# Kernel tuning notes

Measured on AMD Instinct MI355X. Metric: run time of the kernel, lower is better.

## Reference

```python
import jax, jax.numpy as jnp
import numpy as np

N_LSTM = 256
FEAT = 5
BATCH = 65536


def setup_inputs() -> dict:
    key = jax.random.key(0)
    ks = jax.random.split(key, 9)
    s = 1.0 / np.sqrt(N_LSTM)
    return {
        "seq_in": jax.random.normal(ks[0], (BATCH, 1, FEAT), dtype=jnp.float32),
        "h0": jax.random.normal(ks[1], (BATCH, N_LSTM), dtype=jnp.float32) * 0.1,
        "c0": jax.random.normal(ks[2], (BATCH, N_LSTM), dtype=jnp.float32) * 0.1,
        "W": jax.random.normal(ks[3], (FEAT, 4 * N_LSTM), dtype=jnp.float32) * s,
        "U": jax.random.normal(ks[4], (N_LSTM, 4 * N_LSTM), dtype=jnp.float32) * s,
        "b": jnp.zeros((4 * N_LSTM,), dtype=jnp.float32),
        "Wd": jax.random.normal(ks[5], (N_LSTM, 5), dtype=jnp.float32) * s,
        "bd": jnp.zeros((5,), dtype=jnp.float32),
    }


def reference(seq_in, h0, c0, W, U, b, Wd, bd):
    # Single-step Keras LSTM with activation=relu (applied to candidate and
    # cell output), recurrent_activation=sigmoid. Dropout inactive (inference).
    x = seq_in[:, 0, :]                         # [B, FEAT]
    z = x @ W + h0 @ U + b                      # [B, 4*N] fused gate GEMM
    zi, zf, zc, zo = jnp.split(z, 4, axis=-1)
    i = jax.nn.sigmoid(zi)
    f = jax.nn.sigmoid(zf)
    o = jax.nn.sigmoid(zo)
    c = f * c0 + i * jax.nn.relu(zc)            # new cell state
    h = o * jax.nn.relu(c)                      # new hidden state
    logits = h @ Wd + bd                        # [B, 5]
    return (logits, h, c)
```

## Files before the change

kernel.cpp:

```cpp
#include <hip/hip_runtime.h>
#include <hip/hip_bf16.h>

typedef __bf16 bf16x8 __attribute__((ext_vector_type(8)));
typedef float f32x4 __attribute__((ext_vector_type(4)));
typedef unsigned int u32;

#define BATCH 65536
#define NL 256
#define NZ 1024
#define FEAT 5
#define KTOT 288
#define AST 288
#define ROWS 32
#define COLS 64
#define SLAB_T 16
#define NBLK 512
#define TSTR 68
#define FB_ROWS 64
#define FB_COLS 128
#define ASTRIDE 296
#define CSTR 132

__device__ __forceinline__ unsigned short f2bf(float f) {
  __hip_bfloat16 h = __float2bfloat16(f);
  return __builtin_bit_cast(unsigned short, h);
}
__device__ __forceinline__ float sigm(float z) {
  return __builtin_amdgcn_rcpf(1.f + __builtin_amdgcn_exp2f(z * -1.4426950408889634f));
}

#define GLOAD16(g, l)                                                              \
  __builtin_amdgcn_global_load_lds((const __attribute__((address_space(1))) u32*)(g), \
                                   (__attribute__((address_space(3))) u32*)(l), 16, 0, 0)

__global__ __launch_bounds__(256) void k_prep_all(
    const float* __restrict__ h0, const float* __restrict__ x,
    const float* __restrict__ U, const float* __restrict__ W,
    const float* __restrict__ Wd, unsigned short* __restrict__ Abig,
    unsigned short* __restrict__ Ut, unsigned short* __restrict__ WdTg) {
  __shared__ float t[32][33];
  const int tid = threadIdx.x;
  const int bid = blockIdx.x;

  if (bid < 8192) {
    const int row8 = bid * 8;
    const int r = tid >> 5;
    const int c8 = tid & 31;
    const int row = row8 + r;
    const float4 v0 = *reinterpret_cast<const float4*>(h0 + (size_t)row * NL + c8 * 8);
    const float4 v1 = *reinterpret_cast<const float4*>(h0 + (size_t)row * NL + c8 * 8 + 4);
    unsigned short* dst = Abig + (size_t)row * AST + c8 * 8;
    *reinterpret_cast<ushort4*>(dst) = make_ushort4(f2bf(v0.x), f2bf(v0.y), f2bf(v0.z), f2bf(v0.w));
    *reinterpret_cast<ushort4*>(dst + 4) = make_ushort4(f2bf(v1.x), f2bf(v1.y), f2bf(v1.z), f2bf(v1.w));
    if (tid < 32) {
      const int rr = row8 + (tid >> 2);
      const int seg = tid & 3;
      unsigned short vals[8];
#pragma unroll
      for (int e = 0; e < 8; ++e) {
        const int col = seg * 8 + e;
        vals[e] = (col < FEAT) ? f2bf(x[(size_t)rr * FEAT + col]) : (unsigned short)0;
      }
      unsigned short* d2 = Abig + (size_t)rr * AST + 256 + seg * 8;
      *reinterpret_cast<ushort4*>(d2) = make_ushort4(vals[0], vals[1], vals[2], vals[3]);
      *reinterpret_cast<ushort4*>(d2 + 4) = make_ushort4(vals[4], vals[5], vals[6], vals[7]);
    }
  } else if (bid < 8448) {
    const int b2 = bid - 8192;
    const int bk = b2 >> 5;
    const int bn = b2 & 31;
    const int r = tid >> 5;
    const int c = tid & 31;
#pragma unroll
    for (int i = 0; i < 4; ++i)
      t[r + 8 * i][c] = U[(size_t)(bk * 32 + r + 8 * i) * NZ + bn * 32 + c];
    __syncthreads();
#pragma unroll
    for (int i = 0; i < 4; ++i)
      Ut[(size_t)(bn * 32 + r + 8 * i) * KTOT + bk * 32 + c] = f2bf(t[c][r + 8 * i]);
  } else if (bid < 8576) {
    const int idx = (bid - 8448) * 256 + tid;
    const int n = idx >> 5;
    const int cc = idx & 31;
    Ut[(size_t)n * KTOT + 256 + cc] =
        (cc < FEAT) ? f2bf(W[(size_t)cc * NZ + n]) : (unsigned short)0;
  } else {
    const int idx = (bid - 8576) * 256 + tid;
    const int p = idx >> 8;
    const int j = idx & 255;
    WdTg[p * 256 + j] = (p < FEAT) ? f2bf(Wd[(size_t)j * FEAT + p]) : (unsigned short)0;
  }
}

__device__ __forceinline__ void issue_tile(const unsigned short* Abig, const float* c0,
                                           int mt, int cg, int w, int l,
                                           unsigned short* Abuf, float* Cbuf) {
  const char* gA = (const char*)(Abig + (size_t)mt * AST);
  char* lA = (char*)Abuf;
#pragma unroll
  for (int i = 0; i < 5; ++i) {
    const int ii = w + i * 4;
    if (ii < 18) GLOAD16(gA + ii * 1024 + l * 16, lA + ii * 1024);
  }
  const char* gC = (const char*)c0;
  char* lC = (char*)Cbuf;
#pragma unroll
  for (int j = 0; j < 2; ++j) {
    const int jj = w + j * 4;
    const int rr = jj * 4 + (l >> 4);
    GLOAD16(gC + ((size_t)(mt + rr) * NL + cg * COLS) * 4 + (l & 15) * 16, lC + jj * 1024);
  }
}

__global__ __launch_bounds__(256, 2) void k_lstm_p(
    const float* __restrict__ c0, const float* __restrict__ b,
    const float* __restrict__ bd, const unsigned short* __restrict__ Ut,
    const unsigned short* __restrict__ WdTg,
    const unsigned short* __restrict__ Abig, float* __restrict__ out) {
  float* out_logits = out;
  float* out_h = out + (size_t)BATCH * FEAT;
  float* out_c = out_h + (size_t)BATCH * NL;

  __shared__ __align__(16) unsigned short A_sh[2][ROWS * AST];
  __shared__ __align__(16) float C_sh[2][ROWS * COLS];
  __shared__ __align__(16) float t_sh[ROWS * TSTR];

  const int tid = threadIdx.x;
  const int w = tid >> 6;
  const int l = tid & 63;
  const int lrow = l & 15;
  const int lk8 = (l >> 4) * 8;
  const int lq = (l >> 4) * 4;

  const int xcd = (int)blockIdx.x & 7;
  const int gidx = xcd * 64 + ((int)blockIdx.x >> 3);
  const int cg = gidx & 3;
  const int slab = gidx >> 2;
  const int mbase = slab * (ROWS * SLAB_T);

  const int jcol = cg * COLS + w * 16 + lrow;
  const int wcol = w * 16 + lrow;

  float bb[4];
#pragma unroll
  for (int g = 0; g < 4; ++g) bb[g] = b[g * 256 + jcol];
  const unsigned short* bp[4];
#pragma unroll
  for (int g = 0; g < 4; ++g) bp[g] = Ut + (size_t)(g * 256 + jcol) * KTOT + lk8;
  const float bdv = (cg == 0 && lrow < FEAT) ? bd[lrow] : 0.f;

  issue_tile(Abig, c0, mbase, cg, w, l, &A_sh[0][0], &C_sh[0][0]);
  asm volatile("s_waitcnt vmcnt(0)" ::: "memory");
  __syncthreads();

  int cur = 0;
#pragma unroll 1
  for (int t = 0; t < SLAB_T; ++t) {
    const int m0 = mbase + t * ROWS;
    if (t + 1 < SLAB_T)
      issue_tile(Abig, c0, m0 + ROWS, cg, w, l, &A_sh[cur ^ 1][0], &C_sh[cur ^ 1][0]);

    f32x4 acc[2][4];
#pragma unroll
    for (int r = 0; r < 2; ++r)
#pragma unroll
      for (int g = 0; g < 4; ++g) acc[r][g] = (f32x4){0.f, 0.f, 0.f, 0.f};
    const unsigned short* Ab = &A_sh[cur][0];

    bf16x8 bbuf[3][4];
#pragma unroll
    for (int g = 0; g < 4; ++g) bbuf[0][g] = *reinterpret_cast<const bf16x8*>(bp[g]);
#pragma unroll
    for (int g = 0; g < 4; ++g) bbuf[1][g] = *reinterpret_cast<const bf16x8*>(bp[g] + 32);

#pragma unroll
    for (int kk = 0; kk < 9; ++kk) {
      if (kk < 7) {
#pragma unroll
        for (int g = 0; g < 4; ++g)
          bbuf[(kk + 2) % 3][g] = *reinterpret_cast<const bf16x8*>(bp[g] + (kk + 2) * 32);
        __builtin_amdgcn_sched_group_barrier(0x20, 4, 0);
      }
      const bf16x8 af0 = *reinterpret_cast<const bf16x8*>(&Ab[lrow * AST + kk * 32 + lk8]);
      const bf16x8 af1 =
          *reinterpret_cast<const bf16x8*>(&Ab[(16 + lrow) * AST + kk * 32 + lk8]);
      __builtin_amdgcn_sched_group_barrier(0x100, 2, 0);
      __builtin_amdgcn_s_setprio(1);
#pragma unroll
      for (int g = 0; g < 4; ++g) {
        acc[0][g] = __builtin_amdgcn_mfma_f32_16x16x32_bf16(af0, bbuf[kk % 3][g], acc[0][g], 0, 0, 0);
        acc[1][g] = __builtin_amdgcn_mfma_f32_16x16x32_bf16(af1, bbuf[kk % 3][g], acc[1][g], 0, 0, 0);
      }
      __builtin_amdgcn_s_setprio(0);
      __builtin_amdgcn_sched_group_barrier(0x8, 8, 0);
    }

#pragma unroll
    for (int r = 0; r < 2; ++r) {
#pragma unroll
      for (int v = 0; v < 4; ++v) {
        const int mloc = r * 16 + lq + v;
        const float zi = acc[r][0][v] + bb[0];
        const float zf = acc[r][1][v] + bb[1];
        const float zc = acc[r][2][v] + bb[2];
        const float zo = acc[r][3][v] + bb[3];
        const float ig = sigm(zi);
        const float fg = sigm(zf);
        const float og = sigm(zo);
        const float rc = fmaxf(zc, 0.f);
        const float cv = fg * C_sh[cur][mloc * COLS + wcol] + ig * rc;
        const float hv = og * fmaxf(cv, 0.f);
        C_sh[cur][mloc * COLS + wcol] = cv;
        t_sh[mloc * TSTR + wcol] = hv;
      }
    }
    __syncthreads();

#pragma unroll
    for (int it = 0; it < 2; ++it) {
      const int fi = it * 256 + tid;
      const int row = fi >> 4, c4 = fi & 15;
      const float4 hv4 = *reinterpret_cast<const float4*>(&t_sh[row * TSTR + c4 * 4]);
      *reinterpret_cast<float4*>(out_h + (size_t)(m0 + row) * NL + cg * COLS + c4 * 4) = hv4;
      const float4 cv4 = *reinterpret_cast<const float4*>(&C_sh[cur][row * COLS + c4 * 4]);
      *reinterpret_cast<float4*>(out_c + (size_t)(m0 + row) * NL + cg * COLS + c4 * 4) = cv4;
    }
    if (w < 2) {
      f32x4 lacc = (f32x4){0.f, 0.f, 0.f, 0.f};
#pragma unroll
      for (int kk2 = 0; kk2 < 2; ++kk2) {
        const float4 hlo = *reinterpret_cast<const float4*>(
            &t_sh[(w * 16 + lrow) * TSTR + kk2 * 32 + lk8]);
        const float4 hhi = *reinterpret_cast<const float4*>(
            &t_sh[(w * 16 + lrow) * TSTR + kk2 * 32 + lk8 + 4]);
        bf16x8 ah;
        ah[0] = (__bf16)hlo.x; ah[1] = (__bf16)hlo.y;
        ah[2] = (__bf16)hlo.z; ah[3] = (__bf16)hlo.w;
        ah[4] = (__bf16)hhi.x; ah[5] = (__bf16)hhi.y;
        ah[6] = (__bf16)hhi.z; ah[7] = (__bf16)hhi.w;
        const bf16x8 bw = *reinterpret_cast<const bf16x8*>(
            &WdTg[lrow * 256 + cg * COLS + kk2 * 32 + lk8]);
        lacc = __builtin_amdgcn_mfma_f32_16x16x32_bf16(ah, bw, lacc, 0, 0, 0);
      }
      if (lrow < FEAT) {
#pragma unroll
        for (int v = 0; v < 4; ++v)
          atomicAdd(&out_logits[(size_t)(m0 + w * 16 + lq + v) * FEAT + lrow],
                    lacc[v] + bdv);
      }
    }
    asm volatile("s_waitcnt vmcnt(8)" ::: "memory");
    __syncthreads();
    cur ^= 1;
  }
}

__global__ __launch_bounds__(256) void k_prep_fb(const float* __restrict__ U,
                                                 unsigned short* __restrict__ Ut) {
  __shared__ float t[32][33];
  const int bk = blockIdx.x >> 5;
  const int bn = blockIdx.x & 31;
  const int r = threadIdx.x >> 5;
  const int c = threadIdx.x & 31;
#pragma unroll
  for (int i = 0; i < 4; ++i)
    t[r + 8 * i][c] = U[(size_t)(bk * 32 + r + 8 * i) * NZ + bn * 32 + c];
  __syncthreads();
#pragma unroll
  for (int i = 0; i < 4; ++i)
    Ut[(size_t)(bn * 32 + r + 8 * i) * KTOT + bk * 32 + c] = f2bf(t[c][r + 8 * i]);
}
__global__ __launch_bounds__(1024) void k_prepx_fb(const float* __restrict__ W,
                                                   const float* __restrict__ Wd,
                                                   unsigned short* __restrict__ Ut,
                                                   unsigned short* __restrict__ WdTg) {
  const int idx = blockIdx.x * 1024 + threadIdx.x;
  const int n = idx >> 5;
  const int cc = idx & 31;
  Ut[(size_t)n * KTOT + 256 + cc] = (cc < FEAT) ? f2bf(W[(size_t)cc * NZ + n]) : (unsigned short)0;
  if (blockIdx.x < 4) {
    const int p = idx >> 8;
    const int j = idx & 255;
    WdTg[p * 256 + j] = (p < FEAT) ? f2bf(Wd[(size_t)j * FEAT + p]) : (unsigned short)0;
  }
}
__global__ __launch_bounds__(512, 4) void k_lstm_fb(
    const float* __restrict__ x, const float* __restrict__ h0,
    const float* __restrict__ c0, const float* __restrict__ b,
    const float* __restrict__ bd, const unsigned short* __restrict__ Ut,
    const unsigned short* __restrict__ WdTg, float* __restrict__ out) {
  float* out_logits = out;
  float* out_h = out + (size_t)BATCH * FEAT;
  float* out_c = out_h + (size_t)BATCH * NL;
  __shared__ __align__(16) unsigned short A_sh[FB_ROWS * ASTRIDE];
  __shared__ __align__(16) float c0_sh[FB_ROWS * CSTR];
  const int tid = threadIdx.x;
  const int w = tid >> 6;
  const int l = tid & 63;
  const int lrow = l & 15;
  const int lk8 = (l >> 4) * 8;
  const int lq = (l >> 4) * 4;
  const int nb = ((int)blockIdx.x & 7) * 256 + ((int)blockIdx.x >> 3);
  const int cg = nb & 1;
  const int m0 = (nb >> 1) * FB_ROWS;
  const int jcol = cg * FB_COLS + w * 16 + lrow;
  const int wcol = w * 16 + lrow;
  {
    float4 sv[8];
#pragma unroll
    for (int it = 0; it < 8; ++it) {
      const int fi = it * 512 + tid;
      const int row = fi >> 6, c4 = fi & 63;
      sv[it] = *reinterpret_cast<const float4*>(h0 + (size_t)(m0 + row) * NL + c4 * 4);
    }
#pragma unroll
    for (int it = 0; it < 8; ++it) {
      const int fi = it * 512 + tid;
      const int row = fi >> 6, c4 = fi & 63;
      *reinterpret_cast<ushort4*>(&A_sh[row * ASTRIDE + c4 * 4]) =
          make_ushort4(f2bf(sv[it].x), f2bf(sv[it].y), f2bf(sv[it].z), f2bf(sv[it].w));
    }
  }
  {
    float4 cv[4];
#pragma unroll
    for (int it = 0; it < 4; ++it) {
      const int fi = it * 512 + tid;
      const int row = fi >> 5, c4 = fi & 31;
      cv[it] = *reinterpret_cast<const float4*>(c0 + (size_t)(m0 + row) * NL + cg * FB_COLS + c4 * 4);
    }
#pragma unroll
    for (int it = 0; it < 4; ++it) {
      const int fi = it * 512 + tid;
      const int row = fi >> 5, c4 = fi & 31;
      *reinterpret_cast<float4*>(&c0_sh[row * CSTR + c4 * 4]) = cv[it];
    }
  }
#pragma unroll
  for (int it = 0; it < 4; ++it) {
    const int idx = it * 512 + tid;
    const int row = idx >> 5, cc = idx & 31;
    const float xv = (cc < FEAT) ? x[(size_t)(m0 + row) * FEAT + cc] : 0.f;
    A_sh[row * ASTRIDE + 256 + cc] = f2bf(xv);
  }
  __syncthreads();
  float bb[4];
#pragma unroll
  for (int g = 0; g < 4; ++g) bb[g] = b[g * 256 + jcol];
  f32x4 acc[4][4];
#pragma unroll
  for (int r = 0; r < 4; ++r)
#pragma unroll
    for (int g = 0; g < 4; ++g) acc[r][g] = (f32x4){0.f, 0.f, 0.f, 0.f};
  const unsigned short* bp[4];
#pragma unroll
  for (int g = 0; g < 4; ++g) bp[g] = Ut + (size_t)(g * 256 + jcol) * KTOT + lk8;
#pragma unroll
  for (int kk = 0; kk < 9; ++kk) {
    bf16x8 bf[4];
#pragma unroll
    for (int g = 0; g < 4; ++g) bf[g] = *reinterpret_cast<const bf16x8*>(bp[g] + kk * 32);
    bf16x8 af[4];
#pragma unroll
    for (int r = 0; r < 4; ++r)
      af[r] = *reinterpret_cast<const bf16x8*>(&A_sh[(r * 16 + lrow) * ASTRIDE + kk * 32 + lk8]);
#pragma unroll
    for (int g = 0; g < 4; ++g)
#pragma unroll
      for (int r = 0; r < 4; ++r)
        acc[r][g] = __builtin_amdgcn_mfma_f32_16x16x32_bf16(af[r], bf[g], acc[r][g], 0, 0, 0);
  }
  __syncthreads();
  float* t_sh = reinterpret_cast<float*>(A_sh);
#pragma unroll
  for (int r = 0; r < 4; ++r) {
#pragma unroll
    for (int v = 0; v < 4; ++v) {
      const int mloc = r * 16 + lq + v;
      const float zi = acc[r][0][v] + bb[0];
      const float zf = acc[r][1][v] + bb[1];
      const float zc = acc[r][2][v] + bb[2];
      const float zo = acc[r][3][v] + bb[3];
      const float ig = sigm(zi);
      const float fg = sigm(zf);
      const float og = sigm(zo);
      const float rc = fmaxf(zc, 0.f);
      const float cv = fg * c0_sh[mloc * CSTR + wcol] + ig * rc;
      const float hv = og * fmaxf(cv, 0.f);
      c0_sh[mloc * CSTR + wcol] = cv;
      t_sh[mloc * CSTR + wcol] = hv;
    }
  }
  __syncthreads();
#pragma unroll
  for (int it = 0; it < 4; ++it) {
    const int fi = it * 512 + tid;
    const int row = fi >> 5, c4 = fi & 31;
    const float4 hv4 = *reinterpret_cast<const float4*>(&t_sh[row * CSTR + c4 * 4]);
    *reinterpret_cast<float4*>(out_h + (size_t)(m0 + row) * NL + cg * FB_COLS + c4 * 4) = hv4;
    const float4 cv4 = *reinterpret_cast<const float4*>(&c0_sh[row * CSTR + c4 * 4]);
    *reinterpret_cast<float4*>(out_c + (size_t)(m0 + row) * NL + cg * FB_COLS + c4 * 4) = cv4;
  }
  if (w < 4) {
    f32x4 lacc = (f32x4){0.f, 0.f, 0.f, 0.f};
#pragma unroll
    for (int kk2 = 0; kk2 < 4; ++kk2) {
      const float4 hlo = *reinterpret_cast<const float4*>(&t_sh[(w * 16 + lrow) * CSTR + kk2 * 32 + lk8]);
      const float4 hhi = *reinterpret_cast<const float4*>(&t_sh[(w * 16 + lrow) * CSTR + kk2 * 32 + lk8 + 4]);
      bf16x8 ah;
      ah[0] = (__bf16)hlo.x; ah[1] = (__bf16)hlo.y;
      ah[2] = (__bf16)hlo.z; ah[3] = (__bf16)hlo.w;
      ah[4] = (__bf16)hhi.x; ah[5] = (__bf16)hhi.y;
      ah[6] = (__bf16)hhi.z; ah[7] = (__bf16)hhi.w;
      const bf16x8 bw = *reinterpret_cast<const bf16x8*>(&WdTg[lrow * 256 + cg * FB_COLS + kk2 * 32 + lk8]);
      lacc = __builtin_amdgcn_mfma_f32_16x16x32_bf16(ah, bw, lacc, 0, 0, 0);
    }
    if (lrow < FEAT) {
      const float addv = (cg == 0) ? bd[lrow] : 0.f;
#pragma unroll
      for (int v = 0; v < 4; ++v)
        atomicAdd(&out_logits[(size_t)(m0 + w * 16 + lq + v) * FEAT + lrow], lacc[v] + addv);
    }
  }
}

extern "C" void kernel_launch(void* const* d_in, const int* in_sizes, int n_in,
                              void* d_out, int out_size, void* d_ws, size_t ws_size,
                              hipStream_t stream) {
  const float* x = (const float*)d_in[0];
  const float* h0 = (const float*)d_in[1];
  const float* c0 = (const float*)d_in[2];
  const float* W = (const float*)d_in[3];
  const float* U = (const float*)d_in[4];
  const float* b = (const float*)d_in[5];
  const float* Wd = (const float*)d_in[6];
  const float* bd = (const float*)d_in[7];

  unsigned short* Ut = (unsigned short*)d_ws;
  unsigned short* WdTg = Ut + (size_t)NZ * KTOT;
  unsigned short* Abig = WdTg + 16 * 256;
  const size_t need = (size_t)NZ * KTOT * 2 + 16 * 256 * 2 + (size_t)BATCH * AST * 2;

  hipMemsetAsync(d_out, 0, (size_t)BATCH * FEAT * sizeof(float), stream);

  if (ws_size >= need) {
    k_prep_all<<<8592, 256, 0, stream>>>(h0, x, U, W, Wd, Abig, Ut, WdTg);
    k_lstm_p<<<NBLK, 256, 0, stream>>>(c0, b, bd, Ut, WdTg, Abig, (float*)d_out);
  } else {
    k_prep_fb<<<256, 256, 0, stream>>>(U, Ut);
    k_prepx_fb<<<32, 1024, 0, stream>>>(W, Wd, Ut, WdTg);
    k_lstm_fb<<<(BATCH / FB_ROWS) * 2, 512, 0, stream>>>(x, h0, c0, b, bd, Ut, WdTg,
                                                         (float*)d_out);
  }
}
```

Before: 95.63 us.

## Widen LSTM blocks to 512 threads covering 128 columns, load c0 directly

The main LSTM kernel now runs 8 waves per block, each block covering 128 gate columns instead of 64, over half as many row tiles per slab. This halves the number of column groups that reload the same A tile. c0 is now read straight from global memory into registers instead of being staged through LDS with async loads. The logits projection is split across all waves, one MFMA each. The risks are exposed c0 load latency and higher register and LDS pressure under the new launch bounds (512, 4).

```diff
diff --git a/kernel.cpp b/kernel.cpp
--- a/kernel.cpp
+++ b/kernel.cpp
@@ -12,10 +12,10 @@
 #define KTOT 288
 #define AST 288
 #define ROWS 32
-#define COLS 64
-#define SLAB_T 16
+#define COLS 128
+#define SLAB_T 8
 #define NBLK 512
-#define TSTR 68
+#define CH 132
 #define FB_ROWS 64
 #define FB_COLS 128
 #define ASTRIDE 296
@@ -92,27 +92,18 @@
   }
 }
 
-__device__ __forceinline__ void issue_tile(const unsigned short* Abig, const float* c0,
-                                           int mt, int cg, int w, int l,
-                                           unsigned short* Abuf, float* Cbuf) {
+__device__ __forceinline__ void issue_tile(const unsigned short* Abig, int mt,
+                                           int w, int l, unsigned short* Abuf) {
   const char* gA = (const char*)(Abig + (size_t)mt * AST);
   char* lA = (char*)Abuf;
 #pragma unroll
-  for (int i = 0; i < 5; ++i) {
-    const int ii = w + i * 4;
+  for (int i = 0; i < 3; ++i) {
+    const int ii = w + i * 8;
     if (ii < 18) GLOAD16(gA + ii * 1024 + l * 16, lA + ii * 1024);
   }
-  const char* gC = (const char*)c0;
-  char* lC = (char*)Cbuf;
-#pragma unroll
-  for (int j = 0; j < 2; ++j) {
-    const int jj = w + j * 4;
-    const int rr = jj * 4 + (l >> 4);
-    GLOAD16(gC + ((size_t)(mt + rr) * NL + cg * COLS) * 4 + (l & 15) * 16, lC + jj * 1024);
-  }
-}
-
-__global__ __launch_bounds__(256, 2) void k_lstm_p(
+}
+
+__global__ __launch_bounds__(512, 4) void k_lstm_p(
     const float* __restrict__ c0, const float* __restrict__ b,
     const float* __restrict__ bd, const unsigned short* __restrict__ Ut,
     const unsigned short* __restrict__ WdTg,
@@ -122,8 +113,8 @@
   float* out_c = out_h + (size_t)BATCH * NL;
 
   __shared__ __align__(16) unsigned short A_sh[2][ROWS * AST];
-  __shared__ __align__(16) float C_sh[2][ROWS * COLS];
-  __shared__ __align__(16) float t_sh[ROWS * TSTR];
+  __shared__ __align__(16) float c_buf[ROWS * CH];
+  __shared__ __align__(16) float h_buf[ROWS * CH];
 
   const int tid = threadIdx.x;
   const int w = tid >> 6;
@@ -134,8 +125,8 @@
 
   const int xcd = (int)blockIdx.x & 7;
   const int gidx = xcd * 64 + ((int)blockIdx.x >> 3);
-  const int cg = gidx & 3;
-  const int slab = gidx >> 2;
+  const int cg = gidx & 1;
+  const int slab = gidx >> 1;
   const int mbase = slab * (ROWS * SLAB_T);
 
   const int jcol = cg * COLS + w * 16 + lrow;
@@ -147,9 +138,11 @@
   const unsigned short* bp[4];
 #pragma unroll
   for (int g = 0; g < 4; ++g) bp[g] = Ut + (size_t)(g * 256 + jcol) * KTOT + lk8;
-  const float bdv = (cg == 0 && lrow < FEAT) ? bd[lrow] : 0.f;
-
-  issue_tile(Abig, c0, mbase, cg, w, l, &A_sh[0][0], &C_sh[0][0]);
+  const int rows16 = (w & 1) * 16;
+  const int kk2w = w >> 1;
+  const float bdv = (cg == 0 && kk2w == 0 && lrow < FEAT) ? bd[lrow] : 0.f;
+
+  issue_tile(Abig, mbase, w, l, &A_sh[0][0]);
   asm volatile("s_waitcnt vmcnt(0)" ::: "memory");
   __syncthreads();
 
@@ -157,8 +150,14 @@
 #pragma unroll 1
   for (int t = 0; t < SLAB_T; ++t) {
     const int m0 = mbase + t * ROWS;
-    if (t + 1 < SLAB_T)
-      issue_tile(Abig, c0, m0 + ROWS, cg, w, l, &A_sh[cur ^ 1][0], &C_sh[cur ^ 1][0]);
+    if (t + 1 < SLAB_T) issue_tile(Abig, m0 + ROWS, w, l, &A_sh[cur ^ 1][0]);
+
+    float c0v[2][4];
+#pragma unroll
+    for (int r = 0; r < 2; ++r)
+#pragma unroll
+      for (int v = 0; v < 4; ++v)
+        c0v[r][v] = c0[(size_t)(m0 + r * 16 + lq + v) * NL + jcol];
 
     f32x4 acc[2][4];
 #pragma unroll
@@ -208,44 +207,41 @@
         const float fg = sigm(zf);
         const float og = sigm(zo);
         const float rc = fmaxf(zc, 0.f);
-        const float cv = fg * C_sh[cur][mloc * COLS + wcol] + ig * rc;
+        const float cv = fg * c0v[r][v] + ig * rc;
         const float hv = og * fmaxf(cv, 0.f);
-        C_sh[cur][mloc * COLS + wcol] = cv;
-        t_sh[mloc * TSTR + wcol] = hv;
+        c_buf[mloc * CH + wcol] = cv;
+        h_buf[mloc * CH + wcol] = hv;
       }
     }
     __syncthreads();
 
 #pragma unroll
     for (int it = 0; it < 2; ++it) {
-      const int fi = it * 256 + tid;
-      const int row = fi >> 4, c4 = fi & 15;
-      const float4 hv4 = *reinterpret_cast<const float4*>(&t_sh[row * TSTR + c4 * 4]);
+      const int fi = it * 512 + tid;
+      const int row = fi >> 5, c4 = fi & 31;
+      const float4 hv4 = *reinterpret_cast<const float4*>(&h_buf[row * CH + c4 * 4]);
       *reinterpret_cast<float4*>(out_h + (size_t)(m0 + row) * NL + cg * COLS + c4 * 4) = hv4;
-      const float4 cv4 = *reinterpret_cast<const float4*>(&C_sh[cur][row * COLS + c4 * 4]);
+      const float4 cv4 = *reinterpret_cast<const float4*>(&c_buf[row * CH + c4 * 4]);
       *reinterpret_cast<float4*>(out_c + (size_t)(m0 + row) * NL + cg * COLS + c4 * 4) = cv4;
     }
-    if (w < 2) {
+    {
+      const float4 hlo = *reinterpret_cast<const float4*>(
+          &h_buf[(rows16 + lrow) * CH + kk2w * 32 + lk8]);
+      const float4 hhi = *reinterpret_cast<const float4*>(
+          &h_buf[(rows16 + lrow) * CH + kk2w * 32 + lk8 + 4]);
+      bf16x8 ah;
+      ah[0] = (__bf16)hlo.x; ah[1] = (__bf16)hlo.y;
+      ah[2] = (__bf16)hlo.z; ah[3] = (__bf16)hlo.w;
+      ah[4] = (__bf16)hhi.x; ah[5] = (__bf16)hhi.y;
+      ah[6] = (__bf16)hhi.z; ah[7] = (__bf16)hhi.w;
+      const bf16x8 bw = *reinterpret_cast<const bf16x8*>(
+          &WdTg[lrow * 256 + cg * COLS + kk2w * 32 + lk8]);
       f32x4 lacc = (f32x4){0.f, 0.f, 0.f, 0.f};
-#pragma unroll
-      for (int kk2 = 0; kk2 < 2; ++kk2) {
-        const float4 hlo = *reinterpret_cast<const float4*>(
-            &t_sh[(w * 16 + lrow) * TSTR + kk2 * 32 + lk8]);
-        const float4 hhi = *reinterpret_cast<const float4*>(
-            &t_sh[(w * 16 + lrow) * TSTR + kk2 * 32 + lk8 + 4]);
-        bf16x8 ah;
-        ah[0] = (__bf16)hlo.x; ah[1] = (__bf16)hlo.y;
-        ah[2] = (__bf16)hlo.z; ah[3] = (__bf16)hlo.w;
-        ah[4] = (__bf16)hhi.x; ah[5] = (__bf16)hhi.y;
-        ah[6] = (__bf16)hhi.z; ah[7] = (__bf16)hhi.w;
-        const bf16x8 bw = *reinterpret_cast<const bf16x8*>(
-            &WdTg[lrow * 256 + cg * COLS + kk2 * 32 + lk8]);
-        lacc = __builtin_amdgcn_mfma_f32_16x16x32_bf16(ah, bw, lacc, 0, 0, 0);
-      }
+      lacc = __builtin_amdgcn_mfma_f32_16x16x32_bf16(ah, bw, lacc, 0, 0, 0);
       if (lrow < FEAT) {
 #pragma unroll
         for (int v = 0; v < 4; ++v)
-          atomicAdd(&out_logits[(size_t)(m0 + w * 16 + lq + v) * FEAT + lrow],
+          atomicAdd(&out_logits[(size_t)(m0 + rows16 + lq + v) * FEAT + lrow],
                     lacc[v] + bdv);
       }
     }
@@ -445,7 +441,7 @@
 
   if (ws_size >= need) {
     k_prep_all<<<8592, 256, 0, stream>>>(h0, x, U, W, Wd, Abig, Ut, WdTg);
-    k_lstm_p<<<NBLK, 256, 0, stream>>>(c0, b, bd, Ut, WdTg, Abig, (float*)d_out);
+    k_lstm_p<<<NBLK, 512, 0, stream>>>(c0, b, bd, Ut, WdTg, Abig, (float*)d_out);
   } else {
     k_prep_fb<<<256, 256, 0, stream>>>(U, Ut);
     k_prepx_fb<<<32, 1024, 0, stream>>>(W, Wd, Ut, WdTg);
```

Result: slower. 236.8 us (+147.6%).
